# Kernel optimization log

Hardware: AMD Instinct MI355X
Metric: run time of the kernel (lower is better)

The kernel has to match this reference:

```python
import jax, jax.numpy as jnp
import numpy as np

MUL = 128                      # shared multiplicity (MACE channels)
IN_DIMS = (1, 3, 5)            # 0e, 1o, 2e -> d_in_single = 9
OUT_DIMS = (1, 3)              # 0e, 1o -> d_out_single = 4
OUT_SLICES = ((0, 1), (1, 4))
ENTRIES = ((1, 0), (1, 1), (2, 0), (2, 1), (3, 0), (3, 1))  # (nu, out_idx)
N_BASIS = (1, 1, 2, 2, 3, 3)
N_NODES = 2048
N_ELEM = 10


def _to_per_mul(x):
    # (n, sum mul*dim) -> (n, mul, d_in_single)
    n = x.shape[0]
    pieces, off = [], 0
    for d in IN_DIMS:
        pieces.append(x[:, off:off + MUL * d].reshape(n, MUL, d))
        off += MUL * d
    return jnp.concatenate(pieces, axis=-1)


def _from_per_mul(x):
    # (n, mul, d_out_single) -> (n, sum mul*dim)
    n = x.shape[0]
    pieces = []
    for (lo, hi), d in zip(OUT_SLICES, OUT_DIMS):
        pieces.append(x[:, :, lo:hi].reshape(n, MUL * d))
    return jnp.concatenate(pieces, axis=-1)


def _symmetric_contraction(feats, species, bases, weights):
    n = feats.shape[0]
    out = jnp.zeros((n, MUL, sum(OUT_DIMS)), dtype=feats.dtype)
    for (nu, out_idx), basis, w in zip(ENTRIES, bases, weights):
        basis = jax.lax.stop_gradient(basis).astype(feats.dtype)
        # chain of nu symmetric contractions of basis against feats
        tmp = jnp.einsum('a...,ima->im...', basis, feats)  # (n, mul, 9^{nu-1}, nb, d)
        for _ in range(nu - 1):
            tmp = jnp.einsum('ima...,ima->im...', tmp, feats)
        w_per_node = w[species]                           # (n, nb, mul)
        contracted = jnp.einsum('nsm,nmsp->nmp', w_per_node, tmp)
        lo, hi = OUT_SLICES[out_idx]
        out = out.at[:, :, lo:hi].add(contracted)
    return out


def setup_inputs() -> dict:
    key = jax.random.key(0)
    ks = jax.random.split(key, 16)
    d_in = sum(IN_DIMS)
    inp = {
        'node_feats': jax.random.normal(ks[0], (N_NODES, MUL * d_in), jnp.float32),
        'species': jax.random.randint(ks[1], (N_NODES,), 0, N_ELEM),
    }
    names_b = ('b10', 'b11', 'b20', 'b21', 'b30', 'b31')
    names_w = ('w10', 'w11', 'w20', 'w21', 'w30', 'w31')
    for i, ((nu, oi), nb) in enumerate(zip(ENTRIES, N_BASIS)):
        bshape = (d_in,) * nu + (nb, OUT_DIMS[oi])
        inp[names_b[i]] = jax.random.normal(ks[2 + i], bshape, jnp.float32)
        scale = 1.0 / np.sqrt(nb)
        inp[names_w[i]] = jax.random.normal(ks[8 + i], (N_ELEM, nb, MUL), jnp.float32) * scale
    return inp


def reference(node_feats, species, b10, b11, b20, b21, b30, b31,
              w10, w11, w20, w21, w30, w31):
    feats = _to_per_mul(node_feats)
    out = _symmetric_contraction(
        feats, species,
        [b10, b11, b20, b21, b30, b31],
        [w10, w11, w20, w21, w30, w31])
    return _from_per_mul(out)
```

## Files before the change

### kernel.cpp

```cpp
#include <hip/hip_runtime.h>

#define NTH 256
#define RPT 4
#define N_NODES 2048

__global__ __launch_bounds__(NTH, 1) void mace_sc_kernel(
    const float* __restrict__ nf, const int* __restrict__ spec,
    const float* __restrict__ b10, const float* __restrict__ b11,
    const float* __restrict__ b20, const float* __restrict__ b21,
    const float* __restrict__ b30, const float* __restrict__ b31,
    const float* __restrict__ w10, const float* __restrict__ w11,
    const float* __restrict__ w20, const float* __restrict__ w21,
    const float* __restrict__ w30, const float* __restrict__ w31,
    float* __restrict__ out)
{
    __shared__ float l3[165 * 12];
    __shared__ float l2[45 * 8];
    __shared__ float l1[9 * 4];

    const int tid = threadIdx.x;

    if (tid < 165) {
        int i = 0, j = 0, k = 0;
        {
            int c = 0;
            for (int ii = 0; ii < 9; ii++)
                for (int jj = ii; jj < 9; jj++)
                    for (int kk = jj; kk < 9; kk++) {
                        if (c == tid) { i = ii; j = jj; k = kk; }
                        c++;
                    }
        }
        float s[12];
        #pragma unroll
        for (int q = 0; q < 12; q++) s[q] = 0.f;
        auto add3 = [&](int a, int b, int c2) {
            int o30 = ((a * 9 + b) * 9 + c2) * 3;
            int o31 = o30 * 3;
            #pragma unroll
            for (int q = 0; q < 3; q++) s[q] += b30[o30 + q];
            #pragma unroll
            for (int q = 0; q < 9; q++) s[3 + q] += b31[o31 + q];
        };
        if (i == j && j == k) { add3(i, j, k); }
        else if (i == j)      { add3(i, i, k); add3(i, k, i); add3(k, i, i); }
        else if (j == k)      { add3(i, j, j); add3(j, i, j); add3(j, j, i); }
        else { add3(i,j,k); add3(i,k,j); add3(j,i,k); add3(j,k,i); add3(k,i,j); add3(k,j,i); }
        #pragma unroll
        for (int q = 0; q < 12; q++) l3[tid * 12 + q] = s[q];
    } else if (tid < 210) {
        int t = tid - 165;
        int i = 0, j = 0;
        {
            int c = 0;
            for (int ii = 0; ii < 9; ii++)
                for (int jj = ii; jj < 9; jj++) {
                    if (c == t) { i = ii; j = jj; }
                    c++;
                }
        }
        float s[8];
        #pragma unroll
        for (int q = 0; q < 8; q++) s[q] = 0.f;
        auto add2 = [&](int a, int b) {
            int o20 = (a * 9 + b) * 2;
            int o21 = o20 * 3;
            #pragma unroll
            for (int q = 0; q < 2; q++) s[q] += b20[o20 + q];
            #pragma unroll
            for (int q = 0; q < 6; q++) s[2 + q] += b21[o21 + q];
        };
        if (i == j) add2(i, i); else { add2(i, j); add2(j, i); }
        #pragma unroll
        for (int q = 0; q < 8; q++) l2[t * 8 + q] = s[q];
    } else if (tid < 219) {
        int a = tid - 210;
        l1[a * 4 + 0] = b10[a];
        #pragma unroll
        for (int p = 0; p < 3; p++) l1[a * 4 + 1 + p] = b11[a * 3 + p];
    }
    __syncthreads();

    const int g    = blockIdx.x * NTH + tid;
    const int node = g >> 5;
    const int mb   = g & 31;

    const float* nfp = nf + node * 1152;
    float f[RPT][9];
    #pragma unroll
    for (int r = 0; r < RPT; r++) {
        const int m = mb + 32 * r;
        f[r][0] = nfp[m];
        #pragma unroll
        for (int j = 0; j < 3; j++) f[r][1 + j] = nfp[128 + m * 3 + j];
        #pragma unroll
        for (int j = 0; j < 5; j++) f[r][4 + j] = nfp[512 + m * 5 + j];
    }
    const int z = spec[node];

    float acc[RPT][4];
    #pragma unroll
    for (int r = 0; r < RPT; r++)
        #pragma unroll
        for (int p = 0; p < 4; p++) acc[r][p] = 0.f;

    {
        float t3[RPT][12];
        #pragma unroll
        for (int r = 0; r < RPT; r++)
            #pragma unroll
            for (int q = 0; q < 12; q++) t3[r][q] = 0.f;

        int t = 0;
        for (int i = 0; i < 9; i++) {
            for (int j = i; j < 9; j++) {
                float fij[RPT];
                #pragma unroll
                for (int r = 0; r < RPT; r++) fij[r] = f[r][i] * f[r][j];
                for (int k = j; k < 9; k++) {
                    const float* c = &l3[t * 12];
                    float cv[12];
                    #pragma unroll
                    for (int q = 0; q < 12; q++) cv[q] = c[q];
                    #pragma unroll
                    for (int r = 0; r < RPT; r++) {
                        const float m3 = fij[r] * f[r][k];
                        #pragma unroll
                        for (int q = 0; q < 12; q++) t3[r][q] += cv[q] * m3;
                    }
                    t++;
                }
            }
        }
        #pragma unroll
        for (int r = 0; r < RPT; r++) {
            const int m = mb + 32 * r;
            #pragma unroll
            for (int s = 0; s < 3; s++) {
                const float wv = w30[(z * 3 + s) * 128 + m];
                acc[r][0] += wv * t3[r][s];
                const float wu = w31[(z * 3 + s) * 128 + m];
                acc[r][1] += wu * t3[r][3 + s * 3 + 0];
                acc[r][2] += wu * t3[r][3 + s * 3 + 1];
                acc[r][3] += wu * t3[r][3 + s * 3 + 2];
            }
        }
    }

    {
        float t2[RPT][8];
        #pragma unroll
        for (int r = 0; r < RPT; r++)
            #pragma unroll
            for (int q = 0; q < 8; q++) t2[r][q] = 0.f;

        int t = 0;
        for (int i = 0; i < 9; i++) {
            for (int j = i; j < 9; j++) {
                const float* c = &l2[t * 8];
                float cv[8];
                #pragma unroll
                for (int q = 0; q < 8; q++) cv[q] = c[q];
                #pragma unroll
                for (int r = 0; r < RPT; r++) {
                    const float m2 = f[r][i] * f[r][j];
                    #pragma unroll
                    for (int q = 0; q < 8; q++) t2[r][q] += cv[q] * m2;
                }
                t++;
            }
        }
        #pragma unroll
        for (int r = 0; r < RPT; r++) {
            const int m = mb + 32 * r;
            #pragma unroll
            for (int s = 0; s < 2; s++) {
                const float wv = w20[(z * 2 + s) * 128 + m];
                acc[r][0] += wv * t2[r][s];
                const float wu = w21[(z * 2 + s) * 128 + m];
                acc[r][1] += wu * t2[r][2 + s * 3 + 0];
                acc[r][2] += wu * t2[r][2 + s * 3 + 1];
                acc[r][3] += wu * t2[r][2 + s * 3 + 2];
            }
        }
    }

    {
        float t1[RPT][4];
        #pragma unroll
        for (int r = 0; r < RPT; r++)
            #pragma unroll
            for (int q = 0; q < 4; q++) t1[r][q] = 0.f;

        for (int a = 0; a < 9; a++) {
            const float* c = &l1[a * 4];
            float cv[4];
            #pragma unroll
            for (int q = 0; q < 4; q++) cv[q] = c[q];
            #pragma unroll
            for (int r = 0; r < RPT; r++) {
                #pragma unroll
                for (int q = 0; q < 4; q++) t1[r][q] += cv[q] * f[r][a];
            }
        }
        #pragma unroll
        for (int r = 0; r < RPT; r++) {
            const int m = mb + 32 * r;
            const float wv = w10[z * 128 + m];
            acc[r][0] += wv * t1[r][0];
            const float wu = w11[z * 128 + m];
            acc[r][1] += wu * t1[r][1];
            acc[r][2] += wu * t1[r][2];
            acc[r][3] += wu * t1[r][3];
        }
    }

    float* op = out + node * 512;
    #pragma unroll
    for (int r = 0; r < RPT; r++) {
        const int m = mb + 32 * r;
        op[m] = acc[r][0];
        #pragma unroll
        for (int p = 0; p < 3; p++) op[128 + m * 3 + p] = acc[r][1 + p];
    }
}

extern "C" void kernel_launch(void* const* d_in, const int* in_sizes, int n_in,
                              void* d_out, int out_size, void* d_ws, size_t ws_size,
                              hipStream_t stream) {
    const float* nf  = (const float*)d_in[0];
    const int* spec  = (const int*)d_in[1];
    const float* b10 = (const float*)d_in[2];
    const float* w10 = (const float*)d_in[3];
    const float* b11 = (const float*)d_in[4];
    const float* w11 = (const float*)d_in[5];
    const float* b20 = (const float*)d_in[6];
    const float* w20 = (const float*)d_in[7];
    const float* b21 = (const float*)d_in[8];
    const float* w21 = (const float*)d_in[9];
    const float* b30 = (const float*)d_in[10];
    const float* w30 = (const float*)d_in[11];
    const float* b31 = (const float*)d_in[12];
    const float* w31 = (const float*)d_in[13];
    float* out = (float*)d_out;

    const int n_threads = (N_NODES * 128) / RPT;
    const int grid = n_threads / NTH;
    mace_sc_kernel<<<grid, NTH, 0, stream>>>(
        nf, spec, b10, b11, b20, b21, b30, b31,
        w10, w11, w20, w21, w30, w31, out);
}
```

Baseline: 134.1 us.

## Precompute symmetrized basis tables in a prep kernel and fully unroll contractions

Moves the per-block symmetrization of the basis tensors into a separate single-block prep kernel that writes the tables to workspace memory. The main kernel reads those tables from global memory with compile-time-known offsets instead of shared memory. The contraction loops are fully unrolled and use explicit fmaf. Rows per thread drop from 4 to 2 with launch bounds raised to 2 blocks per CU, doubling the grid. This removes the redundant per-block table building and the __syncthreads, at the cost of an extra kernel launch and constant loads served through cache rather than LDS.

```diff
diff --git a/kernel.cpp b/kernel.cpp
--- a/kernel.cpp
+++ b/kernel.cpp
@@ -1,25 +1,21 @@
 #include <hip/hip_runtime.h>
 
 #define NTH 256
-#define RPT 4
+#define RPT 2
 #define N_NODES 2048
 
-__global__ __launch_bounds__(NTH, 1) void mace_sc_kernel(
-    const float* __restrict__ nf, const int* __restrict__ spec,
+#define G3_OFF 0
+#define G2_OFF 1980
+#define G1_OFF 2340
+#define TAB_FLOATS 2376
+
+__global__ void mace_prep(
     const float* __restrict__ b10, const float* __restrict__ b11,
     const float* __restrict__ b20, const float* __restrict__ b21,
     const float* __restrict__ b30, const float* __restrict__ b31,
-    const float* __restrict__ w10, const float* __restrict__ w11,
-    const float* __restrict__ w20, const float* __restrict__ w21,
-    const float* __restrict__ w30, const float* __restrict__ w31,
-    float* __restrict__ out)
+    float* __restrict__ tab)
 {
-    __shared__ float l3[165 * 12];
-    __shared__ float l2[45 * 8];
-    __shared__ float l1[9 * 4];
-
     const int tid = threadIdx.x;
-
     if (tid < 165) {
         int i = 0, j = 0, k = 0;
         {
@@ -47,7 +43,7 @@
         else if (j == k)      { add3(i, j, j); add3(j, i, j); add3(j, j, i); }
         else { add3(i,j,k); add3(i,k,j); add3(j,i,k); add3(j,k,i); add3(k,i,j); add3(k,j,i); }
         #pragma unroll
-        for (int q = 0; q < 12; q++) l3[tid * 12 + q] = s[q];
+        for (int q = 0; q < 12; q++) tab[G3_OFF + tid * 12 + q] = s[q];
     } else if (tid < 210) {
         int t = tid - 165;
         int i = 0, j = 0;
@@ -72,24 +68,31 @@
         };
         if (i == j) add2(i, i); else { add2(i, j); add2(j, i); }
         #pragma unroll
-        for (int q = 0; q < 8; q++) l2[t * 8 + q] = s[q];
+        for (int q = 0; q < 8; q++) tab[G2_OFF + t * 8 + q] = s[q];
     } else if (tid < 219) {
         int a = tid - 210;
-        l1[a * 4 + 0] = b10[a];
-        #pragma unroll
-        for (int p = 0; p < 3; p++) l1[a * 4 + 1 + p] = b11[a * 3 + p];
-    }
-    __syncthreads();
-
-    const int g    = blockIdx.x * NTH + tid;
-    const int node = g >> 5;
-    const int mb   = g & 31;
+        tab[G1_OFF + a * 4 + 0] = b10[a];
+        #pragma unroll
+        for (int p = 0; p < 3; p++) tab[G1_OFF + a * 4 + 1 + p] = b11[a * 3 + p];
+    }
+}
+
+__global__ __launch_bounds__(NTH, 2) void mace_sc_kernel(
+    const float* __restrict__ nf, const int* __restrict__ spec,
+    const float* __restrict__ w10, const float* __restrict__ w11,
+    const float* __restrict__ w20, const float* __restrict__ w21,
+    const float* __restrict__ w30, const float* __restrict__ w31,
+    const float* __restrict__ tab, float* __restrict__ out)
+{
+    const int g    = blockIdx.x * NTH + threadIdx.x;
+    const int node = g >> 6;
+    const int mb   = g & 63;
 
     const float* nfp = nf + node * 1152;
     float f[RPT][9];
     #pragma unroll
     for (int r = 0; r < RPT; r++) {
-        const int m = mb + 32 * r;
+        const int m = mb + 64 * r;
         f[r][0] = nfp[m];
         #pragma unroll
         for (int j = 0; j < 3; j++) f[r][1 + j] = nfp[128 + m * 3 + j];
@@ -112,13 +115,16 @@
             for (int q = 0; q < 12; q++) t3[r][q] = 0.f;
 
         int t = 0;
+        #pragma unroll
         for (int i = 0; i < 9; i++) {
+            #pragma unroll
             for (int j = i; j < 9; j++) {
                 float fij[RPT];
                 #pragma unroll
                 for (int r = 0; r < RPT; r++) fij[r] = f[r][i] * f[r][j];
+                #pragma unroll
                 for (int k = j; k < 9; k++) {
-                    const float* c = &l3[t * 12];
+                    const float* c = &tab[G3_OFF + t * 12];
                     float cv[12];
                     #pragma unroll
                     for (int q = 0; q < 12; q++) cv[q] = c[q];
@@ -126,23 +132,25 @@
                     for (int r = 0; r < RPT; r++) {
                         const float m3 = fij[r] * f[r][k];
                         #pragma unroll
-                        for (int q = 0; q < 12; q++) t3[r][q] += cv[q] * m3;
+                        for (int q = 0; q < 12; q++) t3[r][q] = fmaf(cv[q], m3, t3[r][q]);
                     }
                     t++;
                 }
             }
         }
+        const float* w30z = w30 + z * 3 * 128;
+        const float* w31z = w31 + z * 3 * 128;
         #pragma unroll
         for (int r = 0; r < RPT; r++) {
-            const int m = mb + 32 * r;
+            const int m = mb + 64 * r;
             #pragma unroll
             for (int s = 0; s < 3; s++) {
-                const float wv = w30[(z * 3 + s) * 128 + m];
-                acc[r][0] += wv * t3[r][s];
-                const float wu = w31[(z * 3 + s) * 128 + m];
-                acc[r][1] += wu * t3[r][3 + s * 3 + 0];
-                acc[r][2] += wu * t3[r][3 + s * 3 + 1];
-                acc[r][3] += wu * t3[r][3 + s * 3 + 2];
+                const float wv = w30z[s * 128 + m];
+                acc[r][0] = fmaf(wv, t3[r][s], acc[r][0]);
+                const float wu = w31z[s * 128 + m];
+                acc[r][1] = fmaf(wu, t3[r][3 + s * 3 + 0], acc[r][1]);
+                acc[r][2] = fmaf(wu, t3[r][3 + s * 3 + 1], acc[r][2]);
+                acc[r][3] = fmaf(wu, t3[r][3 + s * 3 + 2], acc[r][3]);
             }
         }
     }
@@ -155,9 +163,11 @@
             for (int q = 0; q < 8; q++) t2[r][q] = 0.f;
 
         int t = 0;
+        #pragma unroll
         for (int i = 0; i < 9; i++) {
+            #pragma unroll
             for (int j = i; j < 9; j++) {
-                const float* c = &l2[t * 8];
+                const float* c = &tab[G2_OFF + t * 8];
                 float cv[8];
                 #pragma unroll
                 for (int q = 0; q < 8; q++) cv[q] = c[q];
@@ -165,22 +175,24 @@
                 for (int r = 0; r < RPT; r++) {
                     const float m2 = f[r][i] * f[r][j];
                     #pragma unroll
-                    for (int q = 0; q < 8; q++) t2[r][q] += cv[q] * m2;
+                    for (int q = 0; q < 8; q++) t2[r][q] = fmaf(cv[q], m2, t2[r][q]);
                 }
                 t++;
             }
         }
+        const float* w20z = w20 + z * 2 * 128;
+        const float* w21z = w21 + z * 2 * 128;
         #pragma unroll
         for (int r = 0; r < RPT; r++) {
-            const int m = mb + 32 * r;
+            const int m = mb + 64 * r;
             #pragma unroll
             for (int s = 0; s < 2; s++) {
-                const float wv = w20[(z * 2 + s) * 128 + m];
-                acc[r][0] += wv * t2[r][s];
-                const float wu = w21[(z * 2 + s) * 128 + m];
-                acc[r][1] += wu * t2[r][2 + s * 3 + 0];
-                acc[r][2] += wu * t2[r][2 + s * 3 + 1];
-                acc[r][3] += wu * t2[r][2 + s * 3 + 2];
+                const float wv = w20z[s * 128 + m];
+                acc[r][0] = fmaf(wv, t2[r][s], acc[r][0]);
+                const float wu = w21z[s * 128 + m];
+                acc[r][1] = fmaf(wu, t2[r][2 + s * 3 + 0], acc[r][1]);
+                acc[r][2] = fmaf(wu, t2[r][2 + s * 3 + 1], acc[r][2]);
+                acc[r][3] = fmaf(wu, t2[r][2 + s * 3 + 2], acc[r][3]);
             }
         }
     }
@@ -192,33 +204,36 @@
             #pragma unroll
             for (int q = 0; q < 4; q++) t1[r][q] = 0.f;
 
+        #pragma unroll
         for (int a = 0; a < 9; a++) {
-            const float* c = &l1[a * 4];
+            const float* c = &tab[G1_OFF + a * 4];
             float cv[4];
             #pragma unroll
             for (int q = 0; q < 4; q++) cv[q] = c[q];
             #pragma unroll
             for (int r = 0; r < RPT; r++) {
                 #pragma unroll
-                for (int q = 0; q < 4; q++) t1[r][q] += cv[q] * f[r][a];
-            }
-        }
+                for (int q = 0; q < 4; q++) t1[r][q] = fmaf(cv[q], f[r][a], t1[r][q]);
+            }
+        }
+        const float* w10z = w10 + z * 128;
+        const float* w11z = w11 + z * 128;
         #pragma unroll
         for (int r = 0; r < RPT; r++) {
-            const int m = mb + 32 * r;
-            const float wv = w10[z * 128 + m];
-            acc[r][0] += wv * t1[r][0];
-            const float wu = w11[z * 128 + m];
-            acc[r][1] += wu * t1[r][1];
-            acc[r][2] += wu * t1[r][2];
-            acc[r][3] += wu * t1[r][3];
+            const int m = mb + 64 * r;
+            const float wv = w10z[m];
+            acc[r][0] = fmaf(wv, t1[r][0], acc[r][0]);
+            const float wu = w11z[m];
+            acc[r][1] = fmaf(wu, t1[r][1], acc[r][1]);
+            acc[r][2] = fmaf(wu, t1[r][2], acc[r][2]);
+            acc[r][3] = fmaf(wu, t1[r][3], acc[r][3]);
         }
     }
 
     float* op = out + node * 512;
     #pragma unroll
     for (int r = 0; r < RPT; r++) {
-        const int m = mb + 32 * r;
+        const int m = mb + 64 * r;
         op[m] = acc[r][0];
         #pragma unroll
         for (int p = 0; p < 3; p++) op[128 + m * 3 + p] = acc[r][1 + p];
@@ -243,10 +258,12 @@
     const float* b31 = (const float*)d_in[12];
     const float* w31 = (const float*)d_in[13];
     float* out = (float*)d_out;
+    float* tab = (float*)d_ws;
+
+    mace_prep<<<1, 256, 0, stream>>>(b10, b11, b20, b21, b30, b31, tab);
 
     const int n_threads = (N_NODES * 128) / RPT;
     const int grid = n_threads / NTH;
     mace_sc_kernel<<<grid, NTH, 0, stream>>>(
-        nf, spec, b10, b11, b20, b21, b30, b31,
-        w10, w11, w20, w21, w30, w31, out);
+        nf, spec, w10, w11, w20, w21, w30, w31, tab, out);
 }
```

New measurement: 119.2 us. 11.1% less time.
